# Kernel optimization log

Hardware: AMD Instinct MI355X
Metric: run time of the kernel (lower is better)

The kernel has to match this reference:

```python
import jax, jax.numpy as jnp
import numpy as np

B = 4           # batchsize == poolsize, pool = arange(B)
N_NODES = 32768
N_EDGES = 262144
CH_V = 16
CH_E = 16
HID = 64
CH_MSG = 2 * CH_V + CH_E  # 48


def setup_inputs() -> dict:
    key = jax.random.key(0)
    ks = jax.random.split(key, 8)
    node_vals = jax.random.normal(ks[0], (B, N_NODES, CH_V), jnp.float32) * 0.01
    edge_vals = jax.random.normal(ks[1], (B, N_EDGES, CH_E), jnp.float32) * 0.1
    conn_a = jax.random.randint(ks[2], (N_EDGES,), 0, N_NODES)
    conn_b = jax.random.randint(ks[3], (N_EDGES,), 0, N_NODES)
    w = lambda k, sh: jax.random.normal(k, sh, jnp.float32) * 0.1
    return {
        "node_vals": node_vals, "edge_vals": edge_vals,
        "conn_a": conn_a, "conn_b": conn_b,
        "Wm1": w(ks[4], (CH_MSG, HID)), "bm1": jnp.zeros((HID,), jnp.float32),
        "Wm2": w(ks[5], (HID, CH_MSG)), "bm2": jnp.zeros((CH_MSG,), jnp.float32),
        "Wu1": w(ks[6], (3 * CH_V, HID)), "bu1": jnp.zeros((HID,), jnp.float32),
        "Wu2": w(ks[7], (HID, CH_V)), "bu2": jnp.zeros((CH_V,), jnp.float32),
    }


def reference(node_vals, edge_vals, conn_a, conn_b,
              Wm1, bm1, Wm2, bm2, Wu1, bu1, Wu2, bu2):
    # NeuralGraph.timestep with node_dropout_p = edge_dropout_p = 0 (masks are identity),
    # use_update=True, average_messages=True, nodes=True, edges=True.
    h_a = node_vals[:, conn_a]                      # [B, E, CH_V] gather at source nodes
    h_b = node_vals[:, conn_b]                      # [B, E, CH_V] gather at target nodes
    h = jnp.concatenate([h_a, h_b, edge_vals], -1)  # [B, E, 48]
    # message MLP (Linear -> tanh -> Linear)
    m = jnp.tanh(h @ Wm1 + bm1) @ Wm2 + bm2         # [B, E, 48]
    m_a = m[..., :CH_V]
    m_b = m[..., CH_V:2 * CH_V]
    m_ab = m[..., 2 * CH_V:]
    # scatter-add aggregation per node (index_add_ along node dim)
    agg_a = jnp.zeros((B, N_NODES, CH_V), m.dtype).at[:, conn_a].add(m_a)
    agg_b = jnp.zeros((B, N_NODES, CH_V), m.dtype).at[:, conn_b].add(m_b)
    # count-based averaging (counts clamped to >= 1, matching the buffer fixup)
    ones = jnp.ones((N_EDGES,), m.dtype)
    cnt_a = jnp.maximum(jax.ops.segment_sum(ones, conn_a, num_segments=N_NODES), 1.0)
    cnt_b = jnp.maximum(jax.ops.segment_sum(ones, conn_b, num_segments=N_NODES), 1.0)
    agg_a = agg_a / cnt_a[None, :, None]
    agg_b = agg_b / cnt_b[None, :, None]
    # update MLP
    u_in = jnp.concatenate([agg_a, agg_b, node_vals], -1)   # [B, N, 48]
    updates = jnp.tanh(u_in @ Wu1 + bu1) @ Wu2 + bu2        # [B, N, CH_V]
    new_node_vals = node_vals + updates
    new_edge_vals = edge_vals + m_ab
    return new_node_vals, new_edge_vals
```

## Files before the change

kernel.cpp:

```cpp
#include <hip/hip_runtime.h>
#include <hip/hip_bf16.h>
#include <cstdint>
#include <cstddef>

#define B 4
#define NN 32768
#define NE 262144
#define CV 16
#define CE 16
#define HID 64
#define CM 48

using frag  = __attribute__((ext_vector_type(8))) short;
using f32x4 = __attribute__((ext_vector_type(4))) float;

__device__ __forceinline__ float fast_tanh(float x) {
    float e = __expf(2.0f * x);
    return 1.0f - 2.0f / (e + 1.0f);
}

__device__ __forceinline__ unsigned short f2bf(float x) {
    union { float f; unsigned u; } v; v.f = x;
    unsigned r = (v.u + 0x7FFFu + ((v.u >> 16) & 1u)) >> 16;
    return (unsigned short)r;
}

__device__ __forceinline__ float bf2f(unsigned short x) {
    union { unsigned u; float f; } v; v.u = ((unsigned)x) << 16;
    return v.f;
}

__device__ __forceinline__ unsigned pk2bf(float lo, float hi) {
    union { __hip_bfloat162 h; unsigned u; } v;
    v.h = __float22bfloat162_rn(make_float2(lo, hi));
    return v.u;
}

__device__ __forceinline__ unsigned swo(int row, int byte_off) {
    return (unsigned)((row << 7) + (byte_off ^ ((row & 7) << 4)));
}

__global__ __launch_bounds__(256) void count_kernel(
    const int* __restrict__ ca, const int* __restrict__ cb,
    int* __restrict__ cnt_a, int* __restrict__ cnt_b,
    int* __restrict__ rank_a, int* __restrict__ rank_b,
    const float* __restrict__ Wm1, const float* __restrict__ bm1,
    const float* __restrict__ Wm2,
    unsigned short* __restrict__ pW1, unsigned short* __restrict__ pW2)
{
    int i = blockIdx.x * 256 + threadIdx.x;
    rank_a[i] = atomicAdd(&cnt_a[ca[i]], 1);
    rank_b[i] = atomicAdd(&cnt_b[cb[i]], 1);

    if (blockIdx.x == 0) {
        for (int x = threadIdx.x; x < 4 * 2 * 64 * 8; x += 256) {
            int j = x & 7, lane = (x >> 3) & 63, ks = (x >> 9) & 1, mt = x >> 10;
            int m = mt * 16 + (lane & 15);
            int k = ks * 32 + (lane >> 4) * 8 + j;
            float w = (k < 48) ? Wm1[k * 64 + m] : (k == 48 ? bm1[m] : 0.0f);
            pW1[x] = f2bf(w);
        }
    } else if (blockIdx.x == 1) {
        for (int x = threadIdx.x; x < 3 * 2 * 64 * 8; x += 256) {
            int j = x & 7, lane = (x >> 3) & 63, ks = (x >> 9) & 1, mt = x >> 10;
            int m = mt * 16 + (lane & 15);
            int k = ks * 32 + (lane >> 4) * 8 + j;
            pW2[x] = f2bf(Wm2[k * 48 + m]);
        }
    }
}

__global__ __launch_bounds__(1024) void scan_kernel(
    const int* __restrict__ cnt_a, int* __restrict__ start_a,
    const int* __restrict__ cnt_b, int* __restrict__ start_b)
{
    const int* cnt = (blockIdx.x == 0) ? cnt_a : cnt_b;
    int* start     = (blockIdx.x == 0) ? start_a : start_b;

    __shared__ int sw[16];
    int t = threadIdx.x;
    int lane = t & 63;
    int wv   = t >> 6;
    int base = t * 32;

    int local[32];
    int sum = 0;
    const int4* p = (const int4*)(cnt + base);
#pragma unroll
    for (int q = 0; q < 8; q++) {
        int4 v = p[q];
        local[q*4+0] = v.x; local[q*4+1] = v.y; local[q*4+2] = v.z; local[q*4+3] = v.w;
        sum += v.x + v.y + v.z + v.w;
    }
    int inc = sum;
#pragma unroll
    for (int off = 1; off < 64; off <<= 1) {
        int u = __shfl_up(inc, off);
        if (lane >= off) inc += u;
    }
    if (lane == 63) sw[wv] = inc;
    __syncthreads();
    if (wv == 0 && lane < 16) {
        int v = sw[lane];
        int i2 = v;
#pragma unroll
        for (int off = 1; off < 16; off <<= 1) {
            int u = __shfl_up(i2, off);
            if (lane >= off) i2 += u;
        }
        sw[lane] = i2 - v;
    }
    __syncthreads();

    int run = sw[wv] + inc - sum;
    int4* ps = (int4*)(start + base);
#pragma unroll
    for (int q = 0; q < 8; q++) {
        int4 o;
        o.x = run; run += local[q*4+0];
        o.y = run; run += local[q*4+1];
        o.z = run; run += local[q*4+2];
        o.w = run; run += local[q*4+3];
        ps[q] = o;
    }
}

__global__ __launch_bounds__(256, 5) void edge_kernel(
    const float* __restrict__ node_vals, const float* __restrict__ edge_vals,
    const int* __restrict__ ca, const int* __restrict__ cb,
    const int* __restrict__ rank_a, const int* __restrict__ rank_b,
    const int* __restrict__ start_a, const int* __restrict__ start_b,
    const unsigned short* __restrict__ pW1, const unsigned short* __restrict__ pW2,
    const float* __restrict__ bm2,
    float* __restrict__ out_edge,
    unsigned short* __restrict__ ma_csr, unsigned short* __restrict__ mb_csr)
{
    __shared__ unsigned short sH[256 * 64];
    char* sB = (char*)sH;

    int t    = threadIdx.x;
    int lane = t & 63;
    int col  = lane & 15;
    int quad = lane >> 4;
    int erow = (t >> 6) * 64;
    int cha  = quad * 4;

    size_t eb = (size_t)blockIdx.x * 256;
    int posx, posy;
    {
        size_t idx = eb + t;
        int e  = (int)(idx & (NE - 1));
        int bb = (int)(idx >> 18);
        int na = ca[e], nb = cb[e];
        posx = start_a[na] + rank_a[e];
        posy = start_b[nb] + rank_b[e];
        float h[48];
        const float4* pA = (const float4*)(node_vals + ((size_t)bb * NN + na) * CV);
        const float4* pB = (const float4*)(node_vals + ((size_t)bb * NN + nb) * CV);
        const float4* pE = (const float4*)(edge_vals + idx * CE);
#pragma unroll
        for (int q = 0; q < 4; q++) {
            float4 va = pA[q];
            h[q*4+0] = va.x; h[q*4+1] = va.y; h[q*4+2] = va.z; h[q*4+3] = va.w;
            float4 vb = pB[q];
            h[16+q*4+0] = vb.x; h[16+q*4+1] = vb.y; h[16+q*4+2] = vb.z; h[16+q*4+3] = vb.w;
            float4 ve = pE[q];
            h[32+q*4+0] = ve.x; h[32+q*4+1] = ve.y; h[32+q*4+2] = ve.z; h[32+q*4+3] = ve.w;
        }
        unsigned pk[32];
#pragma unroll
        for (int q = 0; q < 24; q++) pk[q] = pk2bf(h[2*q], h[2*q+1]);
        pk[24] = 0x3F80u;
#pragma unroll
        for (int q = 25; q < 32; q++) pk[q] = 0;
        const uint4* src = (const uint4*)pk;
#pragma unroll
        for (int q = 0; q < 8; q++)
            *(uint4*)(sB + swo(t, q * 16)) = src[q];
    }
    asm volatile("s_waitcnt lgkmcnt(0)" ::: "memory");

#pragma unroll
    for (int hh = 0; hh < 2; hh++) {
        int r0 = erow + hh * 32 + col;

        frag w1f[4][2];
#pragma unroll
        for (int mt = 0; mt < 4; mt++)
#pragma unroll
            for (int ks = 0; ks < 2; ks++)
                w1f[mt][ks] = *(const frag*)&pW1[(((mt * 2 + ks) * 64) + lane) * 8];

        f32x4 acc1[4][2];
#pragma unroll
        for (int mt = 0; mt < 4; mt++)
#pragma unroll
            for (int n = 0; n < 2; n++) acc1[mt][n] = (f32x4){0.f, 0.f, 0.f, 0.f};

#pragma unroll
        for (int ks = 0; ks < 2; ks++) {
            frag bfr[2];
#pragma unroll
            for (int n = 0; n < 2; n++)
                bfr[n] = *(const frag*)(sB + swo(r0 + n * 16, ks * 64 + quad * 16));
#pragma unroll
            for (int mt = 0; mt < 4; mt++)
#pragma unroll
                for (int n = 0; n < 2; n++)
                    acc1[mt][n] = __builtin_amdgcn_mfma_f32_16x16x32_bf16(
                        w1f[mt][ks], bfr[n], acc1[mt][n], 0, 0, 0);
        }

#pragma unroll
        for (int n = 0; n < 2; n++) {
            int row = r0 + n * 16;
#pragma unroll
            for (int mt = 0; mt < 4; mt++) {
                uint2 w;
                w.x = pk2bf(fast_tanh(acc1[mt][n][0]), fast_tanh(acc1[mt][n][1]));
                w.y = pk2bf(fast_tanh(acc1[mt][n][2]), fast_tanh(acc1[mt][n][3]));
                *(uint2*)(sB + swo(row, mt * 32 + quad * 8)) = w;
            }
        }
        asm volatile("s_waitcnt lgkmcnt(0)" ::: "memory");

        frag w2f[3][2];
#pragma unroll
        for (int mt = 0; mt < 3; mt++)
#pragma unroll
            for (int ks = 0; ks < 2; ks++)
                w2f[mt][ks] = *(const frag*)&pW2[(((mt * 2 + ks) * 64) + lane) * 8];

        f32x4 acc2[3][2];
#pragma unroll
        for (int mt = 0; mt < 3; mt++)
#pragma unroll
            for (int n = 0; n < 2; n++) acc2[mt][n] = (f32x4){0.f, 0.f, 0.f, 0.f};

#pragma unroll
        for (int ks = 0; ks < 2; ks++) {
            frag bfr[2];
#pragma unroll
            for (int n = 0; n < 2; n++)
                bfr[n] = *(const frag*)(sB + swo(r0 + n * 16, ks * 64 + quad * 16));
#pragma unroll
            for (int mt = 0; mt < 3; mt++)
#pragma unroll
                for (int n = 0; n < 2; n++)
                    acc2[mt][n] = __builtin_amdgcn_mfma_f32_16x16x32_bf16(
                        w2f[mt][ks], bfr[n], acc2[mt][n], 0, 0, 0);
        }

        float4 b2e = *(const float4*)&bm2[32 + cha];
#pragma unroll
        for (int n = 0; n < 2; n++) {
            int le = r0 + n * 16;
            size_t o = (eb + le) * CE + cha;
            float4 ev = *(const float4*)&edge_vals[o];
            float4 ov;
            ov.x = ev.x + acc2[2][n][0] + b2e.x;
            ov.y = ev.y + acc2[2][n][1] + b2e.y;
            ov.z = ev.z + acc2[2][n][2] + b2e.z;
            ov.w = ev.w + acc2[2][n][3] + b2e.w;
            *(float4*)&out_edge[o] = ov;
        }

        float4 b2a = *(const float4*)&bm2[cha];
        float4 b2b = *(const float4*)&bm2[16 + cha];
#pragma unroll
        for (int n = 0; n < 2; n++) {
            int row = r0 + n * 16;
            uint2 wa;
            wa.x = pk2bf(acc2[0][n][0] + b2a.x, acc2[0][n][1] + b2a.y);
            wa.y = pk2bf(acc2[0][n][2] + b2a.z, acc2[0][n][3] + b2a.w);
            *(uint2*)(sB + swo(row, quad * 8)) = wa;
            uint2 wb;
            wb.x = pk2bf(acc2[1][n][0] + b2b.x, acc2[1][n][1] + b2b.y);
            wb.y = pk2bf(acc2[1][n][2] + b2b.z, acc2[1][n][3] + b2b.w);
            *(uint2*)(sB + swo(row, 32 + quad * 8)) = wb;
        }
    }
    asm volatile("s_waitcnt lgkmcnt(0)" ::: "memory");

    {
        int bb = (int)((eb + t) >> 18);
        uint4 a0 = *(const uint4*)(sB + swo(t, 0));
        uint4 a1 = *(const uint4*)(sB + swo(t, 16));
        uint4 b0 = *(const uint4*)(sB + swo(t, 32));
        uint4 b1 = *(const uint4*)(sB + swo(t, 48));
        unsigned short* pa = &ma_csr[((size_t)bb * NE + posx) * 16];
        *(uint4*)(pa + 0) = a0;
        *(uint4*)(pa + 8) = a1;
        unsigned short* pb = &mb_csr[((size_t)bb * NE + posy) * 16];
        *(uint4*)(pb + 0) = b0;
        *(uint4*)(pb + 8) = b1;
    }
}

__global__ __launch_bounds__(256) void agg_kernel(
    const unsigned short* __restrict__ ma_csr, const unsigned short* __restrict__ mb_csr,
    const int* __restrict__ start_a, const int* __restrict__ start_b,
    const int* __restrict__ cnt_a, const int* __restrict__ cnt_b,
    float* __restrict__ agg_a, float* __restrict__ agg_b)
{
    int t = threadIdx.x;
    int team = t >> 5;
    int half = (t >> 4) & 1;
    int l16  = t & 15;
    int eoff  = l16 >> 1;
    int chunk = l16 & 1;
    int g = blockIdx.x * 8 + team;
    int n = g & (NN - 1);
    int b = g >> 15;

    const unsigned short* mcsr = half ? mb_csr : ma_csr;
    const int* stp  = half ? start_b : start_a;
    const int* cntp = half ? cnt_b   : cnt_a;
    float* aggp     = half ? agg_b   : agg_a;

    int d = cntp[n];
    int s = stp[n];
    const unsigned short* base = mcsr + ((size_t)b * NE + s) * 16 + chunk * 8;

    float acc[8] = {0.f, 0.f, 0.f, 0.f, 0.f, 0.f, 0.f, 0.f};
    for (int k = eoff; k < d; k += 8) {
        uint4 v = *(const uint4*)(base + (size_t)k * 16);
        acc[0] += bf2f((unsigned short)(v.x & 0xFFFFu));
        acc[1] += bf2f((unsigned short)(v.x >> 16));
        acc[2] += bf2f((unsigned short)(v.y & 0xFFFFu));
        acc[3] += bf2f((unsigned short)(v.y >> 16));
        acc[4] += bf2f((unsigned short)(v.z & 0xFFFFu));
        acc[5] += bf2f((unsigned short)(v.z >> 16));
        acc[6] += bf2f((unsigned short)(v.w & 0xFFFFu));
        acc[7] += bf2f((unsigned short)(v.w >> 16));
    }
#pragma unroll
    for (int m = 2; m <= 8; m <<= 1) {
#pragma unroll
        for (int i = 0; i < 8; i++) acc[i] += __shfl_xor(acc[i], m);
    }

    if (eoff == 0) {
        float inv = 1.0f / (float)max(d, 1);
        float4 r0, r1;
        r0.x = acc[0]*inv; r0.y = acc[1]*inv; r0.z = acc[2]*inv; r0.w = acc[3]*inv;
        r1.x = acc[4]*inv; r1.y = acc[5]*inv; r1.z = acc[6]*inv; r1.w = acc[7]*inv;
        float* dst = &aggp[(size_t)g * CV + chunk * 8];
        *(float4*)(dst + 0) = r0;
        *(float4*)(dst + 4) = r1;
    }
}

__global__ __launch_bounds__(256) void node_kernel(
    const float* __restrict__ node_vals,
    const float* __restrict__ agg_a, const float* __restrict__ agg_b,
    const float* __restrict__ Wu1, const float* __restrict__ bu1,
    const float* __restrict__ Wu2, const float* __restrict__ bu2,
    float* __restrict__ out_node)
{
    __shared__ float sW1[HID * CM];
    __shared__ float sW2[HID * CV];
    __shared__ float sb1[HID];
    __shared__ float sb2[CV];

    int t = threadIdx.x;
    for (int x = t; x < HID * CM; x += 256) {
        int k = x / CM, i = x - k * CM;
        sW1[x] = Wu1[i * HID + k];
    }
    for (int x = t; x < HID * CV; x += 256) sW2[x] = Wu2[x];
    if (t < HID) sb1[t] = bu1[t];
    if (t < CV)  sb2[t] = bu2[t];
    __syncthreads();

    int idx = blockIdx.x * 256 + t;

    float u[CM];
    const float4* pa = (const float4*)(agg_a + (size_t)idx * CV);
    const float4* pb = (const float4*)(agg_b + (size_t)idx * CV);
    const float4* pn = (const float4*)(node_vals + (size_t)idx * CV);
#pragma unroll
    for (int q = 0; q < 4; q++) {
        float4 va = pa[q];
        u[q*4+0] = va.x; u[q*4+1] = va.y; u[q*4+2] = va.z; u[q*4+3] = va.w;
        float4 vb = pb[q];
        u[16+q*4+0] = vb.x; u[16+q*4+1] = vb.y; u[16+q*4+2] = vb.z; u[16+q*4+3] = vb.w;
        float4 vn = pn[q];
        u[32+q*4+0] = vn.x; u[32+q*4+1] = vn.y; u[32+q*4+2] = vn.z; u[32+q*4+3] = vn.w;
    }

    float o[CV];
#pragma unroll
    for (int j = 0; j < CV; j++) o[j] = sb2[j];

    for (int k = 0; k < HID; k++) {
        float acc = sb1[k];
        const float* w1 = &sW1[k * CM];
#pragma unroll
        for (int i = 0; i < CM; i++) acc = fmaf(u[i], w1[i], acc);
        float th = fast_tanh(acc);
        const float* w2 = &sW2[k * CV];
#pragma unroll
        for (int j = 0; j < CV; j++) o[j] = fmaf(th, w2[j], o[j]);
    }

    float4* on = (float4*)(out_node + (size_t)idx * CV);
#pragma unroll
    for (int q = 0; q < 4; q++) {
        on[q] = make_float4(u[32+q*4+0] + o[q*4+0],
                            u[32+q*4+1] + o[q*4+1],
                            u[32+q*4+2] + o[q*4+2],
                            u[32+q*4+3] + o[q*4+3]);
    }
}

extern "C" void kernel_launch(void* const* d_in, const int* in_sizes, int n_in,
                              void* d_out, int out_size, void* d_ws, size_t ws_size,
                              hipStream_t stream) {
    const float* node_vals = (const float*)d_in[0];
    const float* edge_vals = (const float*)d_in[1];
    const int*   ca        = (const int*)d_in[2];
    const int*   cb        = (const int*)d_in[3];
    const float* Wm1 = (const float*)d_in[4];
    const float* bm1 = (const float*)d_in[5];
    const float* Wm2 = (const float*)d_in[6];
    const float* bm2 = (const float*)d_in[7];
    const float* Wu1 = (const float*)d_in[8];
    const float* bu1 = (const float*)d_in[9];
    const float* Wu2 = (const float*)d_in[10];
    const float* bu2 = (const float*)d_in[11];

    float* out_node = (float*)d_out;
    float* out_edge = out_node + (size_t)B * NN * CV;

    unsigned short* ma_csr = (unsigned short*)d_ws;
    unsigned short* mb_csr = ma_csr + (size_t)B * NE * 16;
    float* agg_a = (float*)(mb_csr + (size_t)B * NE * 16);
    float* agg_b = agg_a + (size_t)B * NN * CV;
    int* cnt_a   = (int*)(agg_b + (size_t)B * NN * CV);
    int* cnt_b   = cnt_a + NN;
    int* start_a = cnt_b + NN;
    int* start_b = start_a + NN;
    int* rank_a  = start_b + NN;
    int* rank_b  = rank_a + NE;
    unsigned short* pW1 = (unsigned short*)(rank_b + NE);
    unsigned short* pW2 = pW1 + 4096;

    hipMemsetAsync(cnt_a, 0, 2 * (size_t)NN * sizeof(int), stream);

    count_kernel<<<NE / 256, 256, 0, stream>>>(
        ca, cb, cnt_a, cnt_b, rank_a, rank_b, Wm1, bm1, Wm2, pW1, pW2);
    scan_kernel<<<2, 1024, 0, stream>>>(cnt_a, start_a, cnt_b, start_b);
    edge_kernel<<<(B * NE) / 256, 256, 0, stream>>>(
        node_vals, edge_vals, ca, cb, rank_a, rank_b, start_a, start_b,
        pW1, pW2, bm2, out_edge, ma_csr, mb_csr);
    agg_kernel<<<(B * NN) / 8, 256, 0, stream>>>(
        ma_csr, mb_csr, start_a, start_b, cnt_a, cnt_b, agg_a, agg_b);
    node_kernel<<<(B * NN) / 256, 256, 0, stream>>>(
        node_vals, agg_a, agg_b, Wu1, bu1, Wu2, bu2, out_node);
}
```

Before: 341.8 us.

## Fuse aggregation into node kernel with MFMA update MLP and XCD-aware edge tiling

Removes the separate aggregation kernel: each node thread now reads its CSR message rows itself, averages them, and feeds the result straight into a bf16 MFMA update MLP using weights packed once in the count kernel. This drops the fp32 agg_a/agg_b round trip through global memory and one launch, and replaces the scalar fp32 update MLP with matrix-core math. The edge kernel also remaps block ids so that blocks for the same batch land on paired XCDs, aiming for better cache locality on node gathers. The cost is that per-node aggregation is now serial over the node's degree in one thread, where before 8 lanes shared it, so degree imbalance and uncoalesced reads may hurt. The update MLP also loses precision by running in bf16.

```diff
diff --git a/kernel.cpp b/kernel.cpp
--- a/kernel.cpp
+++ b/kernel.cpp
@@ -40,13 +40,27 @@
     return (unsigned)((row << 7) + (byte_off ^ ((row & 7) << 4)));
 }
 
+__device__ __forceinline__ void acc8(float* a, uint4 v) {
+    a[0] += bf2f((unsigned short)(v.x & 0xFFFFu));
+    a[1] += bf2f((unsigned short)(v.x >> 16));
+    a[2] += bf2f((unsigned short)(v.y & 0xFFFFu));
+    a[3] += bf2f((unsigned short)(v.y >> 16));
+    a[4] += bf2f((unsigned short)(v.z & 0xFFFFu));
+    a[5] += bf2f((unsigned short)(v.z >> 16));
+    a[6] += bf2f((unsigned short)(v.w & 0xFFFFu));
+    a[7] += bf2f((unsigned short)(v.w >> 16));
+}
+
 __global__ __launch_bounds__(256) void count_kernel(
     const int* __restrict__ ca, const int* __restrict__ cb,
     int* __restrict__ cnt_a, int* __restrict__ cnt_b,
     int* __restrict__ rank_a, int* __restrict__ rank_b,
     const float* __restrict__ Wm1, const float* __restrict__ bm1,
     const float* __restrict__ Wm2,
-    unsigned short* __restrict__ pW1, unsigned short* __restrict__ pW2)
+    const float* __restrict__ Wu1, const float* __restrict__ bu1,
+    const float* __restrict__ Wu2,
+    unsigned short* __restrict__ pW1, unsigned short* __restrict__ pW2,
+    unsigned short* __restrict__ pWu1, unsigned short* __restrict__ pWu2)
 {
     int i = blockIdx.x * 256 + threadIdx.x;
     rank_a[i] = atomicAdd(&cnt_a[ca[i]], 1);
@@ -66,6 +80,21 @@
             int m = mt * 16 + (lane & 15);
             int k = ks * 32 + (lane >> 4) * 8 + j;
             pW2[x] = f2bf(Wm2[k * 48 + m]);
+        }
+    } else if (blockIdx.x == 2) {
+        for (int x = threadIdx.x; x < 4 * 2 * 64 * 8; x += 256) {
+            int j = x & 7, lane = (x >> 3) & 63, ks = (x >> 9) & 1, mt = x >> 10;
+            int m = mt * 16 + (lane & 15);
+            int k = ks * 32 + (lane >> 4) * 8 + j;
+            float w = (k < 48) ? Wu1[k * 64 + m] : (k == 48 ? bu1[m] : 0.0f);
+            pWu1[x] = f2bf(w);
+        }
+    } else if (blockIdx.x == 3) {
+        for (int x = threadIdx.x; x < 2 * 64 * 8; x += 256) {
+            int j = x & 7, lane = (x >> 3) & 63, ks = x >> 9;
+            int m = lane & 15;
+            int k = ks * 32 + (lane >> 4) * 8 + j;
+            pWu2[x] = f2bf(Wu2[k * 16 + m]);
         }
     }
 }
@@ -145,12 +174,16 @@
     int erow = (t >> 6) * 64;
     int cha  = quad * 4;
 
-    size_t eb = (size_t)blockIdx.x * 256;
+    int bid  = blockIdx.x;
+    int xcd  = bid & 7;
+    int bb   = xcd >> 1;
+    int tile = ((bid >> 3) << 1) | (xcd & 1);
+    size_t eb = ((size_t)bb << 18) + ((size_t)tile << 8);
+
     int posx, posy;
     {
+        int e  = (tile << 8) + t;
         size_t idx = eb + t;
-        int e  = (int)(idx & (NE - 1));
-        int bb = (int)(idx >> 18);
         int na = ca[e], nb = cb[e];
         posx = start_a[na] + rank_a[e];
         posy = start_b[nb] + rank_b[e];
@@ -283,7 +316,6 @@
     asm volatile("s_waitcnt lgkmcnt(0)" ::: "memory");
 
     {
-        int bb = (int)((eb + t) >> 18);
         uint4 a0 = *(const uint4*)(sB + swo(t, 0));
         uint4 a1 = *(const uint4*)(sB + swo(t, 16));
         uint4 b0 = *(const uint4*)(sB + swo(t, 32));
@@ -297,120 +329,144 @@
     }
 }
 
-__global__ __launch_bounds__(256) void agg_kernel(
+__global__ __launch_bounds__(256) void node_kernel(
+    const float* __restrict__ node_vals,
     const unsigned short* __restrict__ ma_csr, const unsigned short* __restrict__ mb_csr,
     const int* __restrict__ start_a, const int* __restrict__ start_b,
     const int* __restrict__ cnt_a, const int* __restrict__ cnt_b,
-    float* __restrict__ agg_a, float* __restrict__ agg_b)
+    const unsigned short* __restrict__ pWu1, const unsigned short* __restrict__ pWu2,
+    const float* __restrict__ bu2,
+    float* __restrict__ out_node)
 {
-    int t = threadIdx.x;
-    int team = t >> 5;
-    int half = (t >> 4) & 1;
-    int l16  = t & 15;
-    int eoff  = l16 >> 1;
-    int chunk = l16 & 1;
-    int g = blockIdx.x * 8 + team;
+    __shared__ unsigned short sH[256 * 64];
+    char* sB = (char*)sH;
+
+    int t    = threadIdx.x;
+    int lane = t & 63;
+    int col  = lane & 15;
+    int quad = lane >> 4;
+    int erow = (t >> 6) * 64;
+    int cha  = quad * 4;
+
+    int g = blockIdx.x * 256 + t;
     int n = g & (NN - 1);
     int b = g >> 15;
 
-    const unsigned short* mcsr = half ? mb_csr : ma_csr;
-    const int* stp  = half ? start_b : start_a;
-    const int* cntp = half ? cnt_b   : cnt_a;
-    float* aggp     = half ? agg_b   : agg_a;
-
-    int d = cntp[n];
-    int s = stp[n];
-    const unsigned short* base = mcsr + ((size_t)b * NE + s) * 16 + chunk * 8;
-
-    float acc[8] = {0.f, 0.f, 0.f, 0.f, 0.f, 0.f, 0.f, 0.f};
-    for (int k = eoff; k < d; k += 8) {
-        uint4 v = *(const uint4*)(base + (size_t)k * 16);
-        acc[0] += bf2f((unsigned short)(v.x & 0xFFFFu));
-        acc[1] += bf2f((unsigned short)(v.x >> 16));
-        acc[2] += bf2f((unsigned short)(v.y & 0xFFFFu));
-        acc[3] += bf2f((unsigned short)(v.y >> 16));
-        acc[4] += bf2f((unsigned short)(v.z & 0xFFFFu));
-        acc[5] += bf2f((unsigned short)(v.z >> 16));
-        acc[6] += bf2f((unsigned short)(v.w & 0xFFFFu));
-        acc[7] += bf2f((unsigned short)(v.w >> 16));
-    }
-#pragma unroll
-    for (int m = 2; m <= 8; m <<= 1) {
-#pragma unroll
-        for (int i = 0; i < 8; i++) acc[i] += __shfl_xor(acc[i], m);
-    }
-
-    if (eoff == 0) {
-        float inv = 1.0f / (float)max(d, 1);
-        float4 r0, r1;
-        r0.x = acc[0]*inv; r0.y = acc[1]*inv; r0.z = acc[2]*inv; r0.w = acc[3]*inv;
-        r1.x = acc[4]*inv; r1.y = acc[5]*inv; r1.z = acc[6]*inv; r1.w = acc[7]*inv;
-        float* dst = &aggp[(size_t)g * CV + chunk * 8];
-        *(float4*)(dst + 0) = r0;
-        *(float4*)(dst + 4) = r1;
-    }
-}
-
-__global__ __launch_bounds__(256) void node_kernel(
-    const float* __restrict__ node_vals,
-    const float* __restrict__ agg_a, const float* __restrict__ agg_b,
-    const float* __restrict__ Wu1, const float* __restrict__ bu1,
-    const float* __restrict__ Wu2, const float* __restrict__ bu2,
-    float* __restrict__ out_node)
-{
-    __shared__ float sW1[HID * CM];
-    __shared__ float sW2[HID * CV];
-    __shared__ float sb1[HID];
-    __shared__ float sb2[CV];
-
-    int t = threadIdx.x;
-    for (int x = t; x < HID * CM; x += 256) {
-        int k = x / CM, i = x - k * CM;
-        sW1[x] = Wu1[i * HID + k];
-    }
-    for (int x = t; x < HID * CV; x += 256) sW2[x] = Wu2[x];
-    if (t < HID) sb1[t] = bu1[t];
-    if (t < CV)  sb2[t] = bu2[t];
-    __syncthreads();
-
-    int idx = blockIdx.x * 256 + t;
-
-    float u[CM];
-    const float4* pa = (const float4*)(agg_a + (size_t)idx * CV);
-    const float4* pb = (const float4*)(agg_b + (size_t)idx * CV);
-    const float4* pn = (const float4*)(node_vals + (size_t)idx * CV);
-#pragma unroll
-    for (int q = 0; q < 4; q++) {
-        float4 va = pa[q];
-        u[q*4+0] = va.x; u[q*4+1] = va.y; u[q*4+2] = va.z; u[q*4+3] = va.w;
-        float4 vb = pb[q];
-        u[16+q*4+0] = vb.x; u[16+q*4+1] = vb.y; u[16+q*4+2] = vb.z; u[16+q*4+3] = vb.w;
-        float4 vn = pn[q];
-        u[32+q*4+0] = vn.x; u[32+q*4+1] = vn.y; u[32+q*4+2] = vn.z; u[32+q*4+3] = vn.w;
-    }
-
-    float o[CV];
-#pragma unroll
-    for (int j = 0; j < CV; j++) o[j] = sb2[j];
-
-    for (int k = 0; k < HID; k++) {
-        float acc = sb1[k];
-        const float* w1 = &sW1[k * CM];
-#pragma unroll
-        for (int i = 0; i < CM; i++) acc = fmaf(u[i], w1[i], acc);
-        float th = fast_tanh(acc);
-        const float* w2 = &sW2[k * CV];
-#pragma unroll
-        for (int j = 0; j < CV; j++) o[j] = fmaf(th, w2[j], o[j]);
-    }
-
-    float4* on = (float4*)(out_node + (size_t)idx * CV);
-#pragma unroll
-    for (int q = 0; q < 4; q++) {
-        on[q] = make_float4(u[32+q*4+0] + o[q*4+0],
-                            u[32+q*4+1] + o[q*4+1],
-                            u[32+q*4+2] + o[q*4+2],
-                            u[32+q*4+3] + o[q*4+3]);
+    {
+        float ua[16] = {0.f,0.f,0.f,0.f,0.f,0.f,0.f,0.f,0.f,0.f,0.f,0.f,0.f,0.f,0.f,0.f};
+        float ub[16] = {0.f,0.f,0.f,0.f,0.f,0.f,0.f,0.f,0.f,0.f,0.f,0.f,0.f,0.f,0.f,0.f};
+        int da = cnt_a[n], sa = start_a[n];
+        int db = cnt_b[n], sbn = start_b[n];
+        const unsigned short* pa = ma_csr + ((size_t)b * NE + sa) * 16;
+        const unsigned short* pb = mb_csr + ((size_t)b * NE + sbn) * 16;
+        for (int k = 0; k < da; k++) {
+            acc8(&ua[0], *(const uint4*)(pa + (size_t)k * 16));
+            acc8(&ua[8], *(const uint4*)(pa + (size_t)k * 16 + 8));
+        }
+        for (int k = 0; k < db; k++) {
+            acc8(&ub[0], *(const uint4*)(pb + (size_t)k * 16));
+            acc8(&ub[8], *(const uint4*)(pb + (size_t)k * 16 + 8));
+        }
+        float inva = 1.0f / (float)max(da, 1);
+        float invb = 1.0f / (float)max(db, 1);
+
+        float h[48];
+        const float4* pn = (const float4*)(node_vals + (size_t)g * CV);
+#pragma unroll
+        for (int q = 0; q < 16; q++) h[q]      = ua[q] * inva;
+#pragma unroll
+        for (int q = 0; q < 16; q++) h[16 + q] = ub[q] * invb;
+#pragma unroll
+        for (int q = 0; q < 4; q++) {
+            float4 vn = pn[q];
+            h[32+q*4+0] = vn.x; h[32+q*4+1] = vn.y; h[32+q*4+2] = vn.z; h[32+q*4+3] = vn.w;
+        }
+        unsigned pk[32];
+#pragma unroll
+        for (int q = 0; q < 24; q++) pk[q] = pk2bf(h[2*q], h[2*q+1]);
+        pk[24] = 0x3F80u;
+#pragma unroll
+        for (int q = 25; q < 32; q++) pk[q] = 0;
+        const uint4* src = (const uint4*)pk;
+#pragma unroll
+        for (int q = 0; q < 8; q++)
+            *(uint4*)(sB + swo(t, q * 16)) = src[q];
+    }
+    asm volatile("s_waitcnt lgkmcnt(0)" ::: "memory");
+
+    frag w1f[4][2];
+#pragma unroll
+    for (int mt = 0; mt < 4; mt++)
+#pragma unroll
+        for (int ks = 0; ks < 2; ks++)
+            w1f[mt][ks] = *(const frag*)&pWu1[(((mt * 2 + ks) * 64) + lane) * 8];
+
+    f32x4 acc1[4][4];
+#pragma unroll
+    for (int mt = 0; mt < 4; mt++)
+#pragma unroll
+        for (int nt = 0; nt < 4; nt++) acc1[mt][nt] = (f32x4){0.f, 0.f, 0.f, 0.f};
+
+#pragma unroll
+    for (int ks = 0; ks < 2; ks++) {
+        frag bfr[4];
+#pragma unroll
+        for (int nt = 0; nt < 4; nt++)
+            bfr[nt] = *(const frag*)(sB + swo(erow + nt*16 + col, ks * 64 + quad * 16));
+#pragma unroll
+        for (int mt = 0; mt < 4; mt++)
+#pragma unroll
+            for (int nt = 0; nt < 4; nt++)
+                acc1[mt][nt] = __builtin_amdgcn_mfma_f32_16x16x32_bf16(
+                    w1f[mt][ks], bfr[nt], acc1[mt][nt], 0, 0, 0);
+    }
+
+#pragma unroll
+    for (int nt = 0; nt < 4; nt++) {
+        int row = erow + nt*16 + col;
+#pragma unroll
+        for (int mt = 0; mt < 4; mt++) {
+            uint2 w;
+            w.x = pk2bf(fast_tanh(acc1[mt][nt][0]), fast_tanh(acc1[mt][nt][1]));
+            w.y = pk2bf(fast_tanh(acc1[mt][nt][2]), fast_tanh(acc1[mt][nt][3]));
+            *(uint2*)(sB + swo(row, mt * 32 + quad * 8)) = w;
+        }
+    }
+    asm volatile("s_waitcnt lgkmcnt(0)" ::: "memory");
+
+    frag w2f[2];
+#pragma unroll
+    for (int ks = 0; ks < 2; ks++)
+        w2f[ks] = *(const frag*)&pWu2[(ks * 64 + lane) * 8];
+
+    f32x4 acc2[4];
+#pragma unroll
+    for (int nt = 0; nt < 4; nt++) acc2[nt] = (f32x4){0.f, 0.f, 0.f, 0.f};
+
+#pragma unroll
+    for (int ks = 0; ks < 2; ks++) {
+        frag bfr[4];
+#pragma unroll
+        for (int nt = 0; nt < 4; nt++)
+            bfr[nt] = *(const frag*)(sB + swo(erow + nt*16 + col, ks * 64 + quad * 16));
+#pragma unroll
+        for (int nt = 0; nt < 4; nt++)
+            acc2[nt] = __builtin_amdgcn_mfma_f32_16x16x32_bf16(
+                w2f[ks], bfr[nt], acc2[nt], 0, 0, 0);
+    }
+
+    float4 b2 = *(const float4*)&bu2[cha];
+#pragma unroll
+    for (int nt = 0; nt < 4; nt++) {
+        int le = erow + nt*16 + col;
+        size_t o = ((size_t)blockIdx.x * 256 + le) * CV + cha;
+        float4 nv = *(const float4*)&node_vals[o];
+        float4 ov;
+        ov.x = nv.x + acc2[nt][0] + b2.x;
+        ov.y = nv.y + acc2[nt][1] + b2.y;
+        ov.z = nv.z + acc2[nt][2] + b2.z;
+        ov.w = nv.w + acc2[nt][3] + b2.w;
+        *(float4*)&out_node[o] = ov;
     }
 }
 
@@ -435,27 +491,27 @@
 
     unsigned short* ma_csr = (unsigned short*)d_ws;
     unsigned short* mb_csr = ma_csr + (size_t)B * NE * 16;
-    float* agg_a = (float*)(mb_csr + (size_t)B * NE * 16);
-    float* agg_b = agg_a + (size_t)B * NN * CV;
-    int* cnt_a   = (int*)(agg_b + (size_t)B * NN * CV);
+    int* cnt_a   = (int*)(mb_csr + (size_t)B * NE * 16);
     int* cnt_b   = cnt_a + NN;
     int* start_a = cnt_b + NN;
     int* start_b = start_a + NN;
     int* rank_a  = start_b + NN;
     int* rank_b  = rank_a + NE;
-    unsigned short* pW1 = (unsigned short*)(rank_b + NE);
-    unsigned short* pW2 = pW1 + 4096;
+    unsigned short* pW1  = (unsigned short*)(rank_b + NE);
+    unsigned short* pW2  = pW1 + 4096;
+    unsigned short* pWu1 = pW2 + 3072;
+    unsigned short* pWu2 = pWu1 + 4096;
 
     hipMemsetAsync(cnt_a, 0, 2 * (size_t)NN * sizeof(int), stream);
 
     count_kernel<<<NE / 256, 256, 0, stream>>>(
-        ca, cb, cnt_a, cnt_b, rank_a, rank_b, Wm1, bm1, Wm2, pW1, pW2);
+        ca, cb, cnt_a, cnt_b, rank_a, rank_b,
+        Wm1, bm1, Wm2, Wu1, bu1, Wu2, pW1, pW2, pWu1, pWu2);
     scan_kernel<<<2, 1024, 0, stream>>>(cnt_a, start_a, cnt_b, start_b);
     edge_kernel<<<(B * NE) / 256, 256, 0, stream>>>(
         node_vals, edge_vals, ca, cb, rank_a, rank_b, start_a, start_b,
         pW1, pW2, bm2, out_edge, ma_csr, mb_csr);
-    agg_kernel<<<(B * NN) / 8, 256, 0, stream>>>(
-        ma_csr, mb_csr, start_a, start_b, cnt_a, cnt_b, agg_a, agg_b);
     node_kernel<<<(B * NN) / 256, 256, 0, stream>>>(
-        node_vals, agg_a, agg_b, Wu1, bu1, Wu2, bu2, out_node);
-}
+        node_vals, ma_csr, mb_csr, start_a, start_b, cnt_a, cnt_b,
+        pWu1, pWu2, bu2, out_node);
+}
```

New measurement: 316.7 us. -7.4%, faster.
